# Performance work log

Hardware: AMD Instinct MI355X
Metric: run time of the kernel (lower is better)

The kernel has to match this reference:

```python
import jax, jax.numpy as jnp
import numpy as np

GROUP_SIZE = 128


def _dequant_groupwise(values, scales, group_size):
    # values: [rows, cols] int codes; scales: [rows, cols//group_size]
    rows, cols = values.shape
    groups = cols // group_size  # dims chosen to divide evenly (no padding branch)
    v = values.astype(jnp.float32).reshape(rows, groups, group_size)
    return (v * scales[:, :, None]).reshape(rows, cols)


def setup_inputs() -> dict:
    key = jax.random.key(0)
    ks = jax.random.split(key, 8)
    tokens, d_in, d_out, rank = 8192, 4096, 4096, 256
    return {
        "x": jax.random.normal(ks[0], (tokens, d_in), dtype=jnp.float32),
        "q_values": jax.random.randint(ks[1], (d_out, d_in), 0, 16, dtype=jnp.int32),
        "q_scales": jax.random.uniform(ks[2], (d_out, d_in // GROUP_SIZE), dtype=jnp.float32),
        "l_values": jax.random.randint(ks[3], (d_out, rank), 0, 16, dtype=jnp.int32),
        "l_scales": jax.random.uniform(ks[4], (d_out, rank // GROUP_SIZE), dtype=jnp.float32),
        "r_values": jax.random.randint(ks[5], (rank, d_in), 0, 16, dtype=jnp.int32),
        "r_scales": jax.random.uniform(ks[6], (rank, d_in // GROUP_SIZE), dtype=jnp.float32),
        "bias": jax.random.normal(ks[7], (d_out,), dtype=jnp.float32),
    }


def reference(x, q_values, q_scales, l_values, l_scales, r_values, r_scales, bias):
    # Dequantize groupwise int-quantized weights, then y = x @ Q^T + (x @ R^T) @ L^T + b
    q = _dequant_groupwise(q_values, q_scales, GROUP_SIZE)  # [out, in]
    l = _dequant_groupwise(l_values, l_scales, GROUP_SIZE)  # [out, rank]
    r = _dequant_groupwise(r_values, r_scales, GROUP_SIZE)  # [rank, in]
    xr = jnp.einsum('ti,ri->tr', x, r)          # [tokens, rank]
    base = jnp.einsum('ti,oi->to', x, q)        # [tokens, out]
    low_rank = jnp.einsum('tr,or->to', xr, l)   # [tokens, out]
    return base + low_rank + bias
```

## Files before the change

### kernel.cpp

```cpp
#include <hip/hip_runtime.h>
#include <cstdint>
#include <cstddef>

#define BM 128
#define BN 128
#define BK 64

typedef float f32x4 __attribute__((ext_vector_type(4)));
typedef __bf16 bf16x8 __attribute__((ext_vector_type(8)));

__device__ __forceinline__ unsigned short f2bf(float f) {
    unsigned int u = __float_as_uint(f);
    u += 0x7fffu + ((u >> 16) & 1u);
    return (unsigned short)(u >> 16);
}

__device__ __forceinline__ void async_copy16(const void* g, void* l) {
    __builtin_amdgcn_global_load_lds(
        (__attribute__((address_space(1))) void*)(g),
        (__attribute__((address_space(3))) void*)(l), 16, 0, 0);
}


__global__ void cast_x_kernel(const float* __restrict__ x,
                              unsigned short* __restrict__ o, int n8) {
    int i = blockIdx.x * blockDim.x + threadIdx.x;
    if (i >= n8) return;
    const float4* xv = (const float4*)x;
    float4 a = xv[2 * (size_t)i];
    float4 b = xv[2 * (size_t)i + 1];
    union { unsigned short u[8]; uint4 v; } r;
    r.u[0] = f2bf(a.x); r.u[1] = f2bf(a.y); r.u[2] = f2bf(a.z); r.u[3] = f2bf(a.w);
    r.u[4] = f2bf(b.x); r.u[5] = f2bf(b.y); r.u[6] = f2bf(b.z); r.u[7] = f2bf(b.w);
    ((uint4*)o)[i] = r.v;
}

__global__ void dequant_kernel(const int* __restrict__ v,
                               const float* __restrict__ s,
                               unsigned short* __restrict__ o,
                               int colshift, int gpr, int n8) {
    int i = blockIdx.x * blockDim.x + threadIdx.x;
    if (i >= n8) return;
    int e = i * 8;
    int row = e >> colshift;
    int col = e & ((1 << colshift) - 1);
    float sc = s[row * gpr + (col >> 7)];
    int4 a = ((const int4*)v)[2 * (size_t)i];
    int4 b = ((const int4*)v)[2 * (size_t)i + 1];
    union { unsigned short u[8]; uint4 x; } r;
    r.u[0] = f2bf(a.x * sc); r.u[1] = f2bf(a.y * sc);
    r.u[2] = f2bf(a.z * sc); r.u[3] = f2bf(a.w * sc);
    r.u[4] = f2bf(b.x * sc); r.u[5] = f2bf(b.y * sc);
    r.u[6] = f2bf(b.z * sc); r.u[7] = f2bf(b.w * sc);
    ((uint4*)o)[i] = r.x;
}

__global__ void __launch_bounds__(256)
gemm_bt_kernel(const __bf16* __restrict__ A1, int lda1, int k1steps,
               const __bf16* __restrict__ B1,
               const __bf16* __restrict__ A2, int lda2, int k2steps,
               const __bf16* __restrict__ B2,
               const float* __restrict__ bias,
               float* __restrict__ outf,
               unsigned short* __restrict__ outb,
               int ldo) {
    __shared__ __bf16 As[BM * BK];
    __shared__ __bf16 Bs[BN * BK];

    const int tid  = threadIdx.x;
    const int lane = tid & 63;
    const int wave = tid >> 6;
    const int wm = (wave >> 1) * 64;
    const int wn = (wave & 1) * 64;
    const int mBase = blockIdx.y * BM;
    const int nBase = blockIdx.x * BN;
    const int lrow = lane >> 3;
    const int lcol = (((lane & 7) ^ lrow) & 7) * 8;

    f32x4 acc[4][4] = {};

    #pragma unroll 1
    for (int phase = 0; phase < 2; ++phase) {
        const __bf16* A = phase ? A2 : A1;
        const __bf16* B = phase ? B2 : B1;
        const int lda    = phase ? lda2 : lda1;
        const int ksteps = phase ? k2steps : k1steps;

        for (int kt = 0; kt < ksteps; ++kt) {
            const int k0 = kt * BK;
            #pragma unroll
            for (int r = 0; r < 4; ++r) {
                const int chunk = wave * 4 + r;
                const int row = chunk * 8 + lrow;
                async_copy16(A + (size_t)(mBase + row) * lda + (k0 + lcol),
                             &As[chunk * 512]);
                async_copy16(B + (size_t)(nBase + row) * lda + (k0 + lcol),
                             &Bs[chunk * 512]);
            }
            __syncthreads();

            #pragma unroll
            for (int ks = 0; ks < 2; ++ks) {
                const int kofs = ks * 32 + (lane >> 4) * 8;
                const int swz = kofs >> 3;
                bf16x8 af[4], bfr[4];
                #pragma unroll
                for (int i = 0; i < 4; ++i) {
                    const int m = wm + i * 16 + (lane & 15);
                    af[i] = *(const bf16x8*)&As[m * BK + (((swz ^ m) & 7) << 3)];
                }
                #pragma unroll
                for (int j = 0; j < 4; ++j) {
                    const int n = wn + j * 16 + (lane & 15);
                    bfr[j] = *(const bf16x8*)&Bs[n * BK + (((swz ^ n) & 7) << 3)];
                }
                #pragma unroll
                for (int i = 0; i < 4; ++i)
                    #pragma unroll
                    for (int j = 0; j < 4; ++j)
                        acc[i][j] = __builtin_amdgcn_mfma_f32_16x16x32_bf16(
                            af[i], bfr[j], acc[i][j], 0, 0, 0);
            }
            __syncthreads();
        }
    }

    const int cn = lane & 15;
    const int rg = (lane >> 4) * 4;
    if (outf) {
        #pragma unroll
        for (int j = 0; j < 4; ++j) {
            const int o = nBase + wn + j * 16 + cn;
            const float bv = bias[o];
            #pragma unroll
            for (int i = 0; i < 4; ++i) {
                const int t0 = mBase + wm + i * 16 + rg;
                #pragma unroll
                for (int r = 0; r < 4; ++r)
                    outf[(size_t)(t0 + r) * ldo + o] = acc[i][j][r] + bv;
            }
        }
    } else {
        #pragma unroll
        for (int j = 0; j < 4; ++j) {
            const int o = nBase + wn + j * 16 + cn;
            #pragma unroll
            for (int i = 0; i < 4; ++i) {
                const int t0 = mBase + wm + i * 16 + rg;
                #pragma unroll
                for (int r = 0; r < 4; ++r)
                    outb[(size_t)(t0 + r) * ldo + o] = f2bf(acc[i][j][r]);
            }
        }
    }
}


#define SM_OFF(slot_, mat_, half_) ((((slot_) * 2 + (mat_)) * 2 + (half_)) * 8192)

#define MFMA_QUAD(MG, NG, AA, BB)                                           \
    _Pragma("unroll")                                                       \
    for (int m_ = 0; m_ < 4; ++m_)                                          \
        _Pragma("unroll")                                                   \
        for (int n_ = 0; n_ < 2; ++n_)                                      \
            _Pragma("unroll")                                               \
            for (int k_ = 0; k_ < 2; ++k_)                                  \
                acc[(MG)*4 + m_][(NG)*2 + n_] =                             \
                    __builtin_amdgcn_mfma_f32_16x16x32_bf16(                \
                        AA[m_][k_], BB[n_][k_],                             \
                        acc[(MG)*4 + m_][(NG)*2 + n_], 0, 0, 0)

__device__ __forceinline__ void run_pipeline(
    const __bf16* __restrict__ A, const __bf16* __restrict__ B,
    const int lda, const int nt,
    const int mBase, const int nBase,
    const int wave, const int lane, const int wr, const int wc,
    __bf16* smp, f32x4 (&acc)[8][4])
{
    const int lrow  = lane >> 3;
    const int lcol  = (((lane & 7) ^ lrow) & 7) * 8;
    const int soff0 = (wave * 8 + lrow) * lda + lcol;
    const int soff1 = ((wave + 8) * 8 + lrow) * lda + lcol;

    const __bf16* Abase = A + (size_t)mBase * lda;
    const __bf16* Bbase = B + (size_t)nBase * lda;

    const int aoff0 = (lane & 15) * 64 + ((((lane >> 4))     ^ (lane & 7)) * 8);
    const int aoff1 = (lane & 15) * 64 + (((4 + (lane >> 4)) ^ (lane & 7)) * 8);

    const __bf16* Ah0 = smp + SM_OFF(0, 0, wr);
    const __bf16* Ah1 = smp + SM_OFF(1, 0, wr);
    const __bf16* Bh0 = smp + SM_OFF(0, 1, wc >> 1) + (wc & 1) * 4096;
    const __bf16* Bh1 = smp + SM_OFF(1, 1, wc >> 1) + (wc & 1) * 4096;

#define STAGE(base_, half_, tile_, slot_, mat_) do {                         \
        const __bf16* g_ = (base_) + (size_t)((half_) * 128) * lda +         \
                           (size_t)(tile_) * 64;                             \
        __bf16* d_ = smp + SM_OFF(slot_, mat_, half_);                       \
        async_copy16(g_ + soff0, d_ + wave * 512);                           \
        async_copy16(g_ + soff1, d_ + (wave + 8) * 512);                     \
    } while (0)

    STAGE(Bbase, 0, 0, 0, 1);
    STAGE(Bbase, 1, 0, 0, 1);
    STAGE(Abase, 0, 0, 0, 0);
    STAGE(Abase, 1, 0, 0, 0);
    STAGE(Bbase, 0, 1, 1, 1);
    STAGE(Bbase, 1, 1, 1, 1);
    STAGE(Abase, 0, 1, 1, 0);
    asm volatile("s_waitcnt vmcnt(6)" ::: "memory");
    __builtin_amdgcn_s_barrier();

    bf16x8 aR[4][2], bLo[2][2], bHi[2][2];

    const int niter = nt >> 1;
    #pragma unroll 1
    for (int i = 0; i < niter; ++i) {
        const int t1 = 2 * i + 1;
        int p2 = 2 * i + 2; if (p2 >= nt) p2 = nt - 2;
        int p3 = 2 * i + 3; if (p3 >= nt) p3 = nt - 1;

        #pragma unroll
        for (int m = 0; m < 4; ++m) {
            aR[m][0] = *(const bf16x8*)(Ah0 + m * 1024 + aoff0);
            aR[m][1] = *(const bf16x8*)(Ah0 + m * 1024 + aoff1);
        }
        #pragma unroll
        for (int n = 0; n < 2; ++n) {
            bLo[n][0] = *(const bf16x8*)(Bh0 + n * 1024 + aoff0);
            bLo[n][1] = *(const bf16x8*)(Bh0 + n * 1024 + aoff1);
        }
        STAGE(Abase, 1, t1, 1, 0);
        __builtin_amdgcn_s_barrier();
        asm volatile("s_waitcnt lgkmcnt(0)" ::: "memory");
        __builtin_amdgcn_s_setprio(1);
        MFMA_QUAD(0, 0, aR, bLo);
        __builtin_amdgcn_s_setprio(0);
        __builtin_amdgcn_s_barrier();

        #pragma unroll
        for (int n = 0; n < 2; ++n) {
            bHi[n][0] = *(const bf16x8*)(Bh0 + (2 + n) * 1024 + aoff0);
            bHi[n][1] = *(const bf16x8*)(Bh0 + (2 + n) * 1024 + aoff1);
        }
        STAGE(Bbase, 0, p2, 0, 1);
        __builtin_amdgcn_s_barrier();
        asm volatile("s_waitcnt lgkmcnt(0)" ::: "memory");
        __builtin_amdgcn_s_setprio(1);
        MFMA_QUAD(0, 1, aR, bHi);
        __builtin_amdgcn_s_setprio(0);
        __builtin_amdgcn_s_barrier();

        #pragma unroll
        for (int m = 0; m < 4; ++m) {
            aR[m][0] = *(const bf16x8*)(Ah0 + (4 + m) * 1024 + aoff0);
            aR[m][1] = *(const bf16x8*)(Ah0 + (4 + m) * 1024 + aoff1);
        }
        STAGE(Bbase, 1, p2, 0, 1);
        __builtin_amdgcn_s_barrier();
        asm volatile("s_waitcnt lgkmcnt(0)" ::: "memory");
        __builtin_amdgcn_s_setprio(1);
        MFMA_QUAD(1, 1, aR, bHi);
        __builtin_amdgcn_s_setprio(0);
        __builtin_amdgcn_s_barrier();

        STAGE(Abase, 0, p2, 0, 0);
        asm volatile("s_waitcnt vmcnt(6)" ::: "memory");
        __builtin_amdgcn_s_barrier();
        __builtin_amdgcn_s_setprio(1);
        MFMA_QUAD(1, 0, aR, bLo);
        __builtin_amdgcn_s_setprio(0);
        __builtin_amdgcn_s_barrier();

        #pragma unroll
        for (int m = 0; m < 4; ++m) {
            aR[m][0] = *(const bf16x8*)(Ah1 + m * 1024 + aoff0);
            aR[m][1] = *(const bf16x8*)(Ah1 + m * 1024 + aoff1);
        }
        #pragma unroll
        for (int n = 0; n < 2; ++n) {
            bLo[n][0] = *(const bf16x8*)(Bh1 + n * 1024 + aoff0);
            bLo[n][1] = *(const bf16x8*)(Bh1 + n * 1024 + aoff1);
        }
        STAGE(Abase, 1, p2, 0, 0);
        __builtin_amdgcn_s_barrier();
        asm volatile("s_waitcnt lgkmcnt(0)" ::: "memory");
        __builtin_amdgcn_s_setprio(1);
        MFMA_QUAD(0, 0, aR, bLo);
        __builtin_amdgcn_s_setprio(0);
        __builtin_amdgcn_s_barrier();

        #pragma unroll
        for (int n = 0; n < 2; ++n) {
            bHi[n][0] = *(const bf16x8*)(Bh1 + (2 + n) * 1024 + aoff0);
            bHi[n][1] = *(const bf16x8*)(Bh1 + (2 + n) * 1024 + aoff1);
        }
        STAGE(Bbase, 0, p3, 1, 1);
        __builtin_amdgcn_s_barrier();
        asm volatile("s_waitcnt lgkmcnt(0)" ::: "memory");
        __builtin_amdgcn_s_setprio(1);
        MFMA_QUAD(0, 1, aR, bHi);
        __builtin_amdgcn_s_setprio(0);
        __builtin_amdgcn_s_barrier();

        #pragma unroll
        for (int m = 0; m < 4; ++m) {
            aR[m][0] = *(const bf16x8*)(Ah1 + (4 + m) * 1024 + aoff0);
            aR[m][1] = *(const bf16x8*)(Ah1 + (4 + m) * 1024 + aoff1);
        }
        STAGE(Bbase, 1, p3, 1, 1);
        __builtin_amdgcn_s_barrier();
        asm volatile("s_waitcnt lgkmcnt(0)" ::: "memory");
        __builtin_amdgcn_s_setprio(1);
        MFMA_QUAD(1, 1, aR, bHi);
        __builtin_amdgcn_s_setprio(0);
        __builtin_amdgcn_s_barrier();

        STAGE(Abase, 0, p3, 1, 0);
        asm volatile("s_waitcnt vmcnt(6)" ::: "memory");
        __builtin_amdgcn_s_barrier();
        __builtin_amdgcn_s_setprio(1);
        MFMA_QUAD(1, 0, aR, bLo);
        __builtin_amdgcn_s_setprio(0);
        __builtin_amdgcn_s_barrier();
    }

    asm volatile("s_waitcnt vmcnt(0)" ::: "memory");
    __builtin_amdgcn_s_barrier();
#undef STAGE
}

__global__ void __launch_bounds__(512, 2)
gemm256_kernel(const __bf16* __restrict__ A1, const __bf16* __restrict__ B1,
               int lda1, int nt1,
               const __bf16* __restrict__ A2, const __bf16* __restrict__ B2,
               int lda2, int nt2,
               const float* __restrict__ bias, float* __restrict__ out,
               int ldo, int gxlog2) {
    __shared__ __bf16 sm[2][2][2][8192];

    const int tid  = threadIdx.x;
    const int lane = tid & 63;
    const int wave = tid >> 6;
    const int wr = wave >> 2;
    const int wc = wave & 3;

    const int bid = blockIdx.x;
    const int cpx = gridDim.x >> 3;
    const int s   = (bid & 7) * cpx + (bid >> 3);
    const int bx  = s & ((1 << gxlog2) - 1);
    const int by  = s >> gxlog2;
    const int mBase = by * 256;
    const int nBase = bx * 256;

    f32x4 acc[8][4] = {};

    __bf16* smp = &sm[0][0][0][0];
    run_pipeline(A1, B1, lda1, nt1, mBase, nBase, wave, lane, wr, wc, smp, acc);
    run_pipeline(A2, B2, lda2, nt2, mBase, nBase, wave, lane, wr, wc, smp, acc);

    const int cn = lane & 15;
    const int rg = (lane >> 4) * 4;
    const int row0 = mBase + wr * 128 + rg;
    const int col0 = nBase + wc * 64 + cn;
    #pragma unroll
    for (int nf = 0; nf < 4; ++nf) {
        const int o = col0 + nf * 16;
        const float bv = bias[o];
        #pragma unroll
        for (int mf = 0; mf < 8; ++mf) {
            const int t0 = row0 + mf * 16;
            #pragma unroll
            for (int r = 0; r < 4; ++r)
                out[(size_t)(t0 + r) * ldo + o] = acc[mf][nf][r] + bv;
        }
    }
}

extern "C" void kernel_launch(void* const* d_in, const int* in_sizes, int n_in,
                              void* d_out, int out_size, void* d_ws, size_t ws_size,
                              hipStream_t stream) {
    const float* x    = (const float*)d_in[0];
    const int*   qv   = (const int*)d_in[1];
    const float* qs   = (const float*)d_in[2];
    const int*   lv   = (const int*)d_in[3];
    const float* ls   = (const float*)d_in[4];
    const int*   rv   = (const int*)d_in[5];
    const float* rs   = (const float*)d_in[6];
    const float* bias = (const float*)d_in[7];
    float* out = (float*)d_out;

    const int T = 8192, DI = 4096, DO = 4096, R = 256;

    char* ws = (char*)d_ws;
    unsigned short* xb = (unsigned short*)(ws);
    unsigned short* Qd = (unsigned short*)(ws + 67108864);
    unsigned short* Rd = (unsigned short*)(ws + 100663296);
    unsigned short* Ld = (unsigned short*)(ws + 102760448);
    unsigned short* xr = (unsigned short*)(ws + 104857600);

    {
        int n8 = T * DI / 8;
        cast_x_kernel<<<(n8 + 255) / 256, 256, 0, stream>>>(x, xb, n8);
    }
    {
        int n8 = DO * DI / 8;
        dequant_kernel<<<(n8 + 255) / 256, 256, 0, stream>>>(qv, qs, Qd, 12, DI / 128, n8);
    }
    {
        int n8 = DO * R / 8;
        dequant_kernel<<<(n8 + 255) / 256, 256, 0, stream>>>(lv, ls, Ld, 8, R / 128, n8);
    }
    {
        int n8 = R * DI / 8;
        dequant_kernel<<<(n8 + 255) / 256, 256, 0, stream>>>(rv, rs, Rd, 12, DI / 128, n8);
    }
    {
        dim3 g(R / BN, T / BM);
        gemm_bt_kernel<<<g, 256, 0, stream>>>(
            (const __bf16*)xb, DI, DI / BK, (const __bf16*)Rd,
            nullptr, 0, 0, nullptr,
            nullptr, nullptr, xr, R);
    }
    {
        int nblocks = (DO / 256) * (T / 256);
        gemm256_kernel<<<nblocks, 512, 0, stream>>>(
            (const __bf16*)xb, (const __bf16*)Qd, DI, DI / 64,
            (const __bf16*)xr, (const __bf16*)Ld, R, R / 64,
            bias, out, DO, 4 );
    }
}
```

Before: 603.3 us.

## Fold low-rank product into dequantized weight before the main GEMM

Instead of computing x@R^T and then a second GEMM phase over rank, the code now forms W = Q + L@R once (a 4096x4096x256 GEMM fused with Q dequantization) and runs a single x@W^T GEMM. This removes the skinny x@R^T GEMM over all tokens and the extra K=256 phase in the main kernel, replacing them with a smaller weight-side GEMM. R is dequantized transposed so the existing pipeline can consume it. The trade-off is that rounding L@R+Q to bf16 slightly changes numerics compared with accumulating separately.

```diff
diff --git a/kernel.cpp b/kernel.cpp
--- a/kernel.cpp
+++ b/kernel.cpp
@@ -1,10 +1,6 @@
 #include <hip/hip_runtime.h>
 #include <cstdint>
 #include <cstddef>
-
-#define BM 128
-#define BN 128
-#define BK 64
 
 typedef float f32x4 __attribute__((ext_vector_type(4)));
 typedef __bf16 bf16x8 __attribute__((ext_vector_type(8)));
@@ -55,104 +51,21 @@
     ((uint4*)o)[i] = r.x;
 }
 
-__global__ void __launch_bounds__(256)
-gemm_bt_kernel(const __bf16* __restrict__ A1, int lda1, int k1steps,
-               const __bf16* __restrict__ B1,
-               const __bf16* __restrict__ A2, int lda2, int k2steps,
-               const __bf16* __restrict__ B2,
-               const float* __restrict__ bias,
-               float* __restrict__ outf,
-               unsigned short* __restrict__ outb,
-               int ldo) {
-    __shared__ __bf16 As[BM * BK];
-    __shared__ __bf16 Bs[BN * BK];
-
-    const int tid  = threadIdx.x;
-    const int lane = tid & 63;
-    const int wave = tid >> 6;
-    const int wm = (wave >> 1) * 64;
-    const int wn = (wave & 1) * 64;
-    const int mBase = blockIdx.y * BM;
-    const int nBase = blockIdx.x * BN;
-    const int lrow = lane >> 3;
-    const int lcol = (((lane & 7) ^ lrow) & 7) * 8;
-
-    f32x4 acc[4][4] = {};
-
-    #pragma unroll 1
-    for (int phase = 0; phase < 2; ++phase) {
-        const __bf16* A = phase ? A2 : A1;
-        const __bf16* B = phase ? B2 : B1;
-        const int lda    = phase ? lda2 : lda1;
-        const int ksteps = phase ? k2steps : k1steps;
-
-        for (int kt = 0; kt < ksteps; ++kt) {
-            const int k0 = kt * BK;
-            #pragma unroll
-            for (int r = 0; r < 4; ++r) {
-                const int chunk = wave * 4 + r;
-                const int row = chunk * 8 + lrow;
-                async_copy16(A + (size_t)(mBase + row) * lda + (k0 + lcol),
-                             &As[chunk * 512]);
-                async_copy16(B + (size_t)(nBase + row) * lda + (k0 + lcol),
-                             &Bs[chunk * 512]);
-            }
-            __syncthreads();
-
-            #pragma unroll
-            for (int ks = 0; ks < 2; ++ks) {
-                const int kofs = ks * 32 + (lane >> 4) * 8;
-                const int swz = kofs >> 3;
-                bf16x8 af[4], bfr[4];
-                #pragma unroll
-                for (int i = 0; i < 4; ++i) {
-                    const int m = wm + i * 16 + (lane & 15);
-                    af[i] = *(const bf16x8*)&As[m * BK + (((swz ^ m) & 7) << 3)];
-                }
-                #pragma unroll
-                for (int j = 0; j < 4; ++j) {
-                    const int n = wn + j * 16 + (lane & 15);
-                    bfr[j] = *(const bf16x8*)&Bs[n * BK + (((swz ^ n) & 7) << 3)];
-                }
-                #pragma unroll
-                for (int i = 0; i < 4; ++i)
-                    #pragma unroll
-                    for (int j = 0; j < 4; ++j)
-                        acc[i][j] = __builtin_amdgcn_mfma_f32_16x16x32_bf16(
-                            af[i], bfr[j], acc[i][j], 0, 0, 0);
-            }
-            __syncthreads();
-        }
-    }
-
-    const int cn = lane & 15;
-    const int rg = (lane >> 4) * 4;
-    if (outf) {
-        #pragma unroll
-        for (int j = 0; j < 4; ++j) {
-            const int o = nBase + wn + j * 16 + cn;
-            const float bv = bias[o];
-            #pragma unroll
-            for (int i = 0; i < 4; ++i) {
-                const int t0 = mBase + wm + i * 16 + rg;
-                #pragma unroll
-                for (int r = 0; r < 4; ++r)
-                    outf[(size_t)(t0 + r) * ldo + o] = acc[i][j][r] + bv;
-            }
-        }
-    } else {
-        #pragma unroll
-        for (int j = 0; j < 4; ++j) {
-            const int o = nBase + wn + j * 16 + cn;
-            #pragma unroll
-            for (int i = 0; i < 4; ++i) {
-                const int t0 = mBase + wm + i * 16 + rg;
-                #pragma unroll
-                for (int r = 0; r < 4; ++r)
-                    outb[(size_t)(t0 + r) * ldo + o] = f2bf(acc[i][j][r]);
-            }
-        }
-    }
+__global__ void rt_dequant_kernel(const int* __restrict__ v,
+                                  const float* __restrict__ s,
+                                  unsigned short* __restrict__ o) {
+    int g = blockIdx.x * blockDim.x + threadIdx.x;
+    int i  = g & 4095;
+    int r0 = (g >> 12) << 3;
+    int grp = i >> 7;
+    union { unsigned short u[8]; uint4 x; } w;
+    #pragma unroll
+    for (int k = 0; k < 8; ++k) {
+        int r = r0 + k;
+        float sc = s[r * 32 + grp];
+        w.u[k] = f2bf((float)v[(size_t)r * 4096 + i] * sc);
+    }
+    *(uint4*)&o[(size_t)i * 256 + r0] = w.x;
 }
 
 
@@ -331,10 +244,81 @@
 }
 
 __global__ void __launch_bounds__(512, 2)
-gemm256_kernel(const __bf16* __restrict__ A1, const __bf16* __restrict__ B1,
-               int lda1, int nt1,
-               const __bf16* __restrict__ A2, const __bf16* __restrict__ B2,
-               int lda2, int nt2,
+lr_w_kernel(const __bf16* __restrict__ Ld,
+            const __bf16* __restrict__ Rt,
+            const int*   __restrict__ qv,
+            const float* __restrict__ qs,
+            unsigned short* __restrict__ Wp)
+{
+    __shared__ __bf16 sm[2][2][2][8192];
+    const int tid  = threadIdx.x;
+    const int lane = tid & 63;
+    const int wave = tid >> 6;
+    const int wr = wave >> 2;
+    const int wc = wave & 3;
+
+    const int bid = blockIdx.x;
+    const int cpx = gridDim.x >> 3;
+    const int s   = (bid & 7) * cpx + (bid >> 3);
+    const int mBase = (s >> 4) * 256;
+    const int nBase = (s & 15) * 256;
+
+    f32x4 acc[8][4] = {};
+    __bf16* smp = &sm[0][0][0][0];
+    run_pipeline(Ld, Rt, 256, 4, mBase, nBase, wave, lane, wr, wc, smp, acc);
+
+    float* lsm = (float*)smp;
+    const int cn = lane & 15;
+    const int rg = (lane >> 4) * 4;
+
+    #pragma unroll 1
+    for (int h = 0; h < 2; ++h) {
+        #pragma unroll
+        for (int mf4 = 0; mf4 < 4; ++mf4) {
+            const int mf = h * 4 + mf4;
+            #pragma unroll
+            for (int nf = 0; nf < 4; ++nf) {
+                #pragma unroll
+                for (int r = 0; r < 4; ++r) {
+                    const int lrowi = wr * 64 + mf4 * 16 + rg + r;
+                    const int col = (wc * 64 + nf * 16 + cn) ^ (((lrowi >> 2) & 1) << 4);
+                    lsm[lrowi * 256 + col] = acc[mf][nf][r];
+                }
+            }
+        }
+        __syncthreads();
+        #pragma unroll 2
+        for (int it = 0; it < 8; ++it) {
+            const int linear = it * 512 + tid;
+            const int lrowi  = linear >> 5;
+            const int coff   = (linear & 31) * 8;
+            const int grow = mBase + ((lrowi >> 6) * 128) + h * 64 + (lrowi & 63);
+            const int gcol = nBase + coff;
+            const int cswz = (coff * 4) ^ (((lrowi >> 2) & 1) << 6);
+            const float* lp = (const float*)((const char*)lsm + (size_t)lrowi * 1024 + cswz);
+            f32x4 lo = *(const f32x4*)lp;
+            f32x4 hi = *(const f32x4*)(lp + 4);
+            const float sc = qs[grow * 32 + (gcol >> 7)];
+            const int4 qa = *(const int4*)&qv[(size_t)grow * 4096 + gcol];
+            const int4 qb = *(const int4*)&qv[(size_t)grow * 4096 + gcol + 4];
+            union { unsigned short u[8]; uint4 x; } w;
+            w.u[0] = f2bf(qa.x * sc + lo[0]);
+            w.u[1] = f2bf(qa.y * sc + lo[1]);
+            w.u[2] = f2bf(qa.z * sc + lo[2]);
+            w.u[3] = f2bf(qa.w * sc + lo[3]);
+            w.u[4] = f2bf(qb.x * sc + hi[0]);
+            w.u[5] = f2bf(qb.y * sc + hi[1]);
+            w.u[6] = f2bf(qb.z * sc + hi[2]);
+            w.u[7] = f2bf(qb.w * sc + hi[3]);
+            *(uint4*)&Wp[(size_t)grow * 4096 + gcol] = w.x;
+        }
+        __syncthreads();
+    }
+}
+
+__global__ void __launch_bounds__(512, 2)
+gemm256_kernel(const __bf16* __restrict__ A, const __bf16* __restrict__ B,
+               int lda, int nt,
                const float* __restrict__ bias, float* __restrict__ out,
                int ldo, int gxlog2) {
     __shared__ __bf16 sm[2][2][2][8192];
@@ -354,10 +338,8 @@
     const int nBase = bx * 256;
 
     f32x4 acc[8][4] = {};
-
     __bf16* smp = &sm[0][0][0][0];
-    run_pipeline(A1, B1, lda1, nt1, mBase, nBase, wave, lane, wr, wc, smp, acc);
-    run_pipeline(A2, B2, lda2, nt2, mBase, nBase, wave, lane, wr, wc, smp, acc);
+    run_pipeline(A, B, lda, nt, mBase, nBase, wave, lane, wr, wc, smp, acc);
 
     const int cn = lane & 15;
     const int rg = (lane >> 4) * 4;
@@ -394,39 +376,29 @@
 
     char* ws = (char*)d_ws;
     unsigned short* xb = (unsigned short*)(ws);
-    unsigned short* Qd = (unsigned short*)(ws + 67108864);
-    unsigned short* Rd = (unsigned short*)(ws + 100663296);
-    unsigned short* Ld = (unsigned short*)(ws + 102760448);
-    unsigned short* xr = (unsigned short*)(ws + 104857600);
+    unsigned short* Wp = (unsigned short*)(ws + 67108864);
+    unsigned short* Ld = (unsigned short*)(ws + 100663296);
+    unsigned short* Rt = (unsigned short*)(ws + 102760448);
 
     {
         int n8 = T * DI / 8;
         cast_x_kernel<<<(n8 + 255) / 256, 256, 0, stream>>>(x, xb, n8);
     }
     {
-        int n8 = DO * DI / 8;
-        dequant_kernel<<<(n8 + 255) / 256, 256, 0, stream>>>(qv, qs, Qd, 12, DI / 128, n8);
-    }
-    {
         int n8 = DO * R / 8;
         dequant_kernel<<<(n8 + 255) / 256, 256, 0, stream>>>(lv, ls, Ld, 8, R / 128, n8);
     }
     {
-        int n8 = R * DI / 8;
-        dequant_kernel<<<(n8 + 255) / 256, 256, 0, stream>>>(rv, rs, Rd, 12, DI / 128, n8);
+        rt_dequant_kernel<<<512, 256, 0, stream>>>(rv, rs, Rt);
     }
     {
-        dim3 g(R / BN, T / BM);
-        gemm_bt_kernel<<<g, 256, 0, stream>>>(
-            (const __bf16*)xb, DI, DI / BK, (const __bf16*)Rd,
-            nullptr, 0, 0, nullptr,
-            nullptr, nullptr, xr, R);
+        lr_w_kernel<<<256, 512, 0, stream>>>(
+            (const __bf16*)Ld, (const __bf16*)Rt, qv, qs, Wp);
     }
     {
         int nblocks = (DO / 256) * (T / 256);
         gemm256_kernel<<<nblocks, 512, 0, stream>>>(
-            (const __bf16*)xb, (const __bf16*)Qd, DI, DI / 64,
-            (const __bf16*)xr, (const __bf16*)Ld, R, R / 64,
+            (const __bf16*)xb, (const __bf16*)Wp, DI, DI / 64,
             bias, out, DO, 4 );
     }
 }
```

New measurement: 550.1 us. -8.8%, faster.
